# Performance work log

Hardware: AMD Instinct MI355X
Metric: run time of the kernel (lower is better)

The kernel has to match this reference:

```python
import jax, jax.numpy as jnp
import numpy as np

WH, WW = 16, 16
NUM_HEADS = 16
DIM = 1024
BATCH = 64
SEQ = WH * WW + 1  # 257, includes cls token
NUM_REL = (2 * WH - 1) * (2 * WW - 1) + 3  # 964


def _make_rel_pos_index(wh, ww):
    # BEiT relative position index construction (intended semantics of the torch code)
    coords = np.stack(np.meshgrid(np.arange(wh), np.arange(ww), indexing='ij'))  # [2, wh, ww]
    flat = coords.reshape(2, -1)  # [2, wh*ww]
    rel = flat[:, :, None] - flat[:, None, :]  # [2, N-1, N-1]
    rel = rel.transpose(1, 2, 0).astype(np.int64)
    rel[:, :, 0] += wh - 1
    rel[:, :, 1] += ww - 1
    rel[:, :, 0] *= 2 * ww - 1
    num_rel = (2 * wh - 1) * (2 * ww - 1) + 3
    idx = np.zeros((wh * ww + 1, wh * ww + 1), dtype=np.int32)
    idx[1:, 1:] = rel.sum(-1)
    idx[0, :] = num_rel - 3  # cls-to-token
    idx[:, 0] = num_rel - 2  # token-to-cls
    idx[0, 0] = num_rel - 1  # cls-to-cls
    return idx


def setup_inputs() -> dict:
    key = jax.random.key(0)
    ks = jax.random.split(key, 7)
    return {
        'x': jax.random.normal(ks[0], (BATCH, SEQ, DIM), dtype=jnp.float32),
        'qkv_weight': jax.random.normal(ks[1], (3 * DIM, DIM), dtype=jnp.float32) * 0.02,
        'query_bias': jax.random.normal(ks[2], (DIM,), dtype=jnp.float32) * 0.02,
        'value_bias': jax.random.normal(ks[3], (DIM,), dtype=jnp.float32) * 0.02,
        'rel_pos_bias_table': jax.random.normal(ks[4], (NUM_REL, NUM_HEADS), dtype=jnp.float32) * 0.02,
        'proj_weight': jax.random.normal(ks[5], (DIM, DIM), dtype=jnp.float32) * 0.02,
        'proj_bias': jax.random.normal(ks[6], (DIM,), dtype=jnp.float32) * 0.02,
        'rel_pos_index': jnp.asarray(_make_rel_pos_index(WH, WW)),
    }


def reference(x, qkv_weight, query_bias, value_bias, rel_pos_bias_table,
              proj_weight, proj_bias, rel_pos_index):
    B, N, C = x.shape
    H = rel_pos_bias_table.shape[-1]
    D = qkv_weight.shape[0] // 3 // H
    scale = D ** -0.5
    # qkv bias: (q_bias, zeros, v_bias) as in the torch module
    qkv_bias = jnp.concatenate([query_bias, jnp.zeros_like(value_bias), value_bias])
    qkv = x @ qkv_weight.T + qkv_bias  # [B, N, 3*H*D]
    qkv = qkv.reshape(B, N, 3, H, D).transpose(2, 0, 3, 1, 4)  # [3, B, H, N, D]
    q, k, v = qkv[0] * scale, qkv[1], qkv[2]
    attn = jnp.einsum('bhqd,bhkd->bhqk', q, k)  # [B, H, N, N]
    bias = rel_pos_bias_table[rel_pos_index]  # [N, N, H]
    attn = attn + bias.transpose(2, 0, 1)[None]  # add per-head bias
    attn = jax.nn.softmax(attn, axis=-1)
    out = jnp.einsum('bhqk,bhkd->bhqd', attn, v)  # [B, H, N, D]
    out = out.transpose(0, 2, 1, 3).reshape(B, N, H * D)
    return out @ proj_weight.T + proj_bias
```

## Files before the change

### kernel.cpp

```cpp
#include <hip/hip_runtime.h>


typedef unsigned short u16;
typedef __attribute__((ext_vector_type(8))) short bf16x8;
typedef __attribute__((ext_vector_type(4))) float f32x4;

#define MFMA16(a, b, c) __builtin_amdgcn_mfma_f32_16x16x32_bf16(a, b, c, 0, 0, 0)
#define GLDS16(g, l)                                                           \
  __builtin_amdgcn_global_load_lds(                                            \
      (const __attribute__((address_space(1))) void*)(g),                      \
      (__attribute__((address_space(3))) void*)(l), 16, 0, 0)

#define QOFF 0
#define KOFF 16842752
#define VTOFF 33685504
#define VTP 264

__device__ __forceinline__ u16 f2bf(float f) {
  unsigned u = __builtin_bit_cast(unsigned, f);
  u += 0x7FFFu + ((u >> 16) & 1u);
  return (u16)(u >> 16);
}
__device__ __forceinline__ unsigned pack2(float a, float b) {
  return (unsigned)f2bf(a) | ((unsigned)f2bf(b) << 16);
}

__global__ __launch_bounds__(256) void cvt_bf16(const float* __restrict__ in,
                                                u16* __restrict__ out, int n4) {
  int i = blockIdx.x * 256 + threadIdx.x;
  if (i < n4) {
    float4 v = ((const float4*)in)[i];
    uint2 o;
    o.x = pack2(v.x, v.y);
    o.y = pack2(v.z, v.w);
    ((uint2*)out)[i] = o;
  }
}

__global__ __launch_bounds__(256) void bias_pre(const float* __restrict__ tab,
                                                const int* __restrict__ idx,
                                                float* __restrict__ out) {
  int t = blockIdx.x * 256 + threadIdx.x;
  if (t < 66049) {
    int id = idx[t];
    const float* row = tab + (size_t)id * 16;
#pragma unroll
    for (int h = 0; h < 16; h++)
      out[(size_t)h * 66049 + t] = row[h] * 1.4426950408889634f;
  }
}


#define GEMM_PROLOG(M_, K_)                                                    \
  __shared__ __align__(16) u16 As[128 * 32];                                   \
  __shared__ __align__(16) u16 Bs[128 * 32];                                   \
  const int M = (M_), K = (K_);                                                \
  const int tid = threadIdx.x;                                                 \
  const int lane = tid & 63, wave = tid >> 6;                                  \
  const int quad = lane >> 4, l15 = lane & 15;                                 \
  const int wr = (wave >> 1) * 64, wc = (wave & 1) * 64;                       \
  const int m0 = blockIdx.y * 128, n0 = blockIdx.x * 128;                      \
  const int sgk = (((tid & 3) ^ ((tid >> 3) & 3))) * 8;  \
  const int fo = ((quad ^ ((l15 >> 1) & 3))) * 8;         \
  int ar0 = m0 + (tid >> 2); if (ar0 > M - 1) ar0 = M - 1;                     \
  int ar1 = m0 + 64 + (tid >> 2); if (ar1 > M - 1) ar1 = M - 1;                \
  const u16* pa0 = A + (size_t)ar0 * K + sgk;                                  \
  const u16* pa1 = A + (size_t)ar1 * K + sgk;                                  \
  const u16* pb0 = B + (size_t)(n0 + (tid >> 2)) * K + sgk;                    \
  const u16* pb1 = pb0 + (size_t)64 * K;                                       \
  f32x4 acc[4][4];                                                             \
  _Pragma("unroll") for (int i = 0; i < 4; i++)                                \
  _Pragma("unroll") for (int j = 0; j < 4; j++)                                \
      acc[i][j] = (f32x4){0.f, 0.f, 0.f, 0.f};                                 \
  for (int k0 = 0; k0 < K; k0 += 32) {                                         \
    __syncthreads();                                                           \
    GLDS16(pa0 + k0, As + tid * 8);                                            \
    GLDS16(pa1 + k0, As + 2048 + tid * 8);                                     \
    GLDS16(pb0 + k0, Bs + tid * 8);                                            \
    GLDS16(pb1 + k0, Bs + 2048 + tid * 8);                                     \
    __syncthreads();                                                           \
    bf16x8 af[4], bf[4];                                                       \
    _Pragma("unroll") for (int t = 0; t < 4; t++)                              \
        af[t] = *(const bf16x8*)(As + (wr + t * 16 + l15) * 32 + fo);          \
    _Pragma("unroll") for (int t = 0; t < 4; t++)                              \
        bf[t] = *(const bf16x8*)(Bs + (wc + t * 16 + l15) * 32 + fo);          \
    _Pragma("unroll") for (int i = 0; i < 4; i++)                              \
    _Pragma("unroll") for (int j = 0; j < 4; j++)                              \
        acc[i][j] = MFMA16(af[i], bf[j], acc[i][j]);                           \
  }

__global__ __launch_bounds__(256) void gemm_qkv(
    const u16* __restrict__ A, const u16* __restrict__ B,
    const float* __restrict__ qbias, const float* __restrict__ vbias,
    u16* __restrict__ C) {
  GEMM_PROLOG(16448, 1024)
#pragma unroll
  for (int i = 0; i < 4; i++) {
#pragma unroll
    for (int r = 0; r < 4; r++) {
      int row = m0 + wr + i * 16 + quad * 4 + r;
      if (row < M) {
        unsigned bb = (unsigned)row / 257u;
        unsigned nn = (unsigned)row - bb * 257u;
#pragma unroll
        for (int j = 0; j < 4; j++) {
          int c = n0 + wc + j * 16 + l15;
          int which = c >> 10, rem = c & 1023;
          float bias = (which == 0) ? qbias[rem]
                                    : ((which == 2) ? vbias[rem] : 0.f);
          float v = acc[i][j][r] + bias;
          if (which == 0) v *= 0.18033688011112042f;
          int h = rem >> 6, d = rem & 63;
          size_t dst;
          if (which == 2) {
            dst = (size_t)VTOFF + ((size_t)(bb * 16 + h) * 64 + d) * VTP + nn;
          } else {
            dst = (size_t)which * 16842752 + (size_t)(bb * 16 + h) * 16448 +
                  (size_t)nn * 64 + d;
          }
          C[dst] = f2bf(v);
        }
      }
    }
  }
}

__global__ __launch_bounds__(256) void gemm_proj(
    const u16* __restrict__ A, const u16* __restrict__ B,
    const float* __restrict__ pbias, float* __restrict__ C) {
  GEMM_PROLOG(16448, 1024)
#pragma unroll
  for (int i = 0; i < 4; i++) {
#pragma unroll
    for (int r = 0; r < 4; r++) {
      int row = m0 + wr + i * 16 + quad * 4 + r;
      if (row < M) {
#pragma unroll
        for (int j = 0; j < 4; j++) {
          int c = n0 + wc + j * 16 + l15;
          C[(size_t)row * 1024 + c] = acc[i][j][r] + pbias[c];
        }
      }
    }
  }
}

__global__ __launch_bounds__(256, 3) void attn_fused(
    const u16* __restrict__ qkv, const float* __restrict__ biasT,
    u16* __restrict__ out) {
  __shared__ __align__(16) u16 KVs[96 * 72];
  __shared__ __align__(16) u16 Ps[4 * 16 * 104];
  const int bx = blockIdx.x;
  const int qt = bx % 5, bh = bx / 5;
  const int b = bh >> 4, h = bh & 15;
  const int tid = threadIdx.x, lane = tid & 63, wave = tid >> 6;
  const int quad = lane >> 4, l15 = lane & 15;
  const u16* qg = qkv + QOFF + (size_t)bh * 16448;
  const u16* kg = qkv + KOFF + (size_t)bh * 16448;
  const u16* vtg = qkv + VTOFF + (size_t)bh * (64 * VTP);

  int qra = qt * 64 + wave * 16 + l15;
  if (qra > 256) qra = 256;
  const bf16x8 aq0 = *(const bf16x8*)(qg + (size_t)qra * 64 + quad * 8);
  const bf16x8 aq1 = *(const bf16x8*)(qg + (size_t)qra * 64 + 32 + quad * 8);

  const int qbase = qt * 64 + wave * 16 + quad * 4;
  const float* bb = biasT + (size_t)h * 66049;
  f32x4 s[18];
#pragma unroll
  for (int r = 0; r < 4; r++) {
    int qr = qbase + r;
    if (qr > 256) qr = 256;
    const float* brow = bb + (size_t)qr * 257;
#pragma unroll
    for (int t = 0; t < 18; t++) {
      int kc = t * 16 + l15;
      s[t][r] = (kc < 257) ? brow[kc] : -3e38f;
    }
  }

  const bf16x8 zv = {0, 0, 0, 0, 0, 0, 0, 0};
  for (int ck = 0; ck < 3; ck++) {
    __syncthreads();
#pragma unroll
    for (int it = 0; it < 3; it++) {
      int g = it * 256 + tid;
      int row = g >> 3, col = (g & 7) * 8;
      int gr = ck * 96 + row;
      bf16x8 kv = (gr < 257) ? *(const bf16x8*)(kg + (size_t)gr * 64 + col) : zv;
      *(bf16x8*)(KVs + row * 72 + col) = kv;
    }
    __syncthreads();
#pragma unroll
    for (int nt = 0; nt < 6; nt++) {
      bf16x8 b0 = *(const bf16x8*)(KVs + (nt * 16 + l15) * 72 + quad * 8);
      bf16x8 b1 = *(const bf16x8*)(KVs + (nt * 16 + l15) * 72 + 32 + quad * 8);
      int t = ck * 6 + nt;
      s[t] = MFMA16(aq0, b0, s[t]);
      s[t] = MFMA16(aq1, b1, s[t]);
    }
  }

  float inv[4];
#pragma unroll
  for (int r = 0; r < 4; r++) {
    float m = -3e38f;
#pragma unroll
    for (int t = 0; t < 18; t++) m = fmaxf(m, s[t][r]);
    m = fmaxf(m, __shfl_xor(m, 1));
    m = fmaxf(m, __shfl_xor(m, 2));
    m = fmaxf(m, __shfl_xor(m, 4));
    m = fmaxf(m, __shfl_xor(m, 8));
    float sum = 0.f;
#pragma unroll
    for (int t = 0; t < 18; t++) {
      float p = __builtin_amdgcn_exp2f(s[t][r] - m);
      s[t][r] = p;
      sum += p;
    }
    sum += __shfl_xor(sum, 1);
    sum += __shfl_xor(sum, 2);
    sum += __shfl_xor(sum, 4);
    sum += __shfl_xor(sum, 8);
    inv[r] = 1.f / sum;
  }

  u16* Pw = Ps + wave * (16 * 104);
  f32x4 o[4];
#pragma unroll
  for (int nt = 0; nt < 4; nt++) o[nt] = (f32x4){0.f, 0.f, 0.f, 0.f};
  for (int ck = 0; ck < 3; ck++) {
    __syncthreads();
#pragma unroll
    for (int it = 0; it < 3; it++) {
      int g = it * 256 + tid;
      int row = g / 12, c = (g % 12) * 8;
      bf16x8 v = *(const bf16x8*)(vtg + (size_t)row * VTP + ck * 96 + c);
      *(bf16x8*)(KVs + row * 104 + c) = v;
    }
#pragma unroll
    for (int nt = 0; nt < 6; nt++) {
      int t = ck * 6 + nt;
#pragma unroll
      for (int r = 0; r < 4; r++)
        Pw[(quad * 4 + r) * 104 + nt * 16 + l15] = f2bf(s[t][r]);
    }
    __syncthreads();
#pragma unroll
    for (int ks = 0; ks < 3; ks++) {
      bf16x8 ap = *(const bf16x8*)(Pw + l15 * 104 + ks * 32 + quad * 8);
#pragma unroll
      for (int nt = 0; nt < 4; nt++) {
        bf16x8 bv =
            *(const bf16x8*)(KVs + (nt * 16 + l15) * 104 + ks * 32 + quad * 8);
        o[nt] = MFMA16(ap, bv, o[nt]);
      }
    }
  }

#pragma unroll
  for (int nt = 0; nt < 4; nt++) {
    int d = nt * 16 + l15;
#pragma unroll
    for (int r = 0; r < 4; r++) {
      int qr = qbase + r;
      if (qr < 257)
        out[((size_t)b * 257 + qr) * 1024 + h * 64 + d] =
            f2bf(o[nt][r] * inv[r]);
    }
  }
}

extern "C" void kernel_launch(void* const* d_in, const int* in_sizes, int n_in,
                              void* d_out, int out_size, void* d_ws,
                              size_t ws_size, hipStream_t stream) {
  const float* x = (const float*)d_in[0];
  const float* qkvw = (const float*)d_in[1];
  const float* qb = (const float*)d_in[2];
  const float* vb = (const float*)d_in[3];
  const float* tab = (const float*)d_in[4];
  const float* pw = (const float*)d_in[5];
  const float* pb = (const float*)d_in[6];
  const int* rpi = (const int*)d_in[7];

  char* ws = (char*)d_ws;
  u16* qkvbuf = (u16*)ws;
  u16* xbuf = (u16*)(ws + 101974016);
  float* biasb = (float*)(ws + 135659520);
  u16* qkvwb = (u16*)(ws + 139886656);
  u16* projwb = (u16*)(ws + 146178112);

  cvt_bf16<<<16448, 256, 0, stream>>>(x, xbuf, 4210688);
  cvt_bf16<<<3072, 256, 0, stream>>>(qkvw, qkvwb, 786432);
  cvt_bf16<<<1024, 256, 0, stream>>>(pw, projwb, 262144);
  bias_pre<<<259, 256, 0, stream>>>(tab, rpi, biasb);
  gemm_qkv<<<dim3(24, 129), 256, 0, stream>>>(xbuf, qkvwb, qb, vb, qkvbuf);
  attn_fused<<<5120, 256, 0, stream>>>(qkvbuf, biasb, xbuf);
  gemm_proj<<<dim3(8, 129), 256, 0, stream>>>(xbuf, projwb, pb, (float*)d_out);
}
```

Measured before the change: 466.1 us.

## Double-buffer LDS tiles in QKV and projection GEMMs to overlap loads with MFMA

The shared GEMM main loop now uses two LDS buffers per operand. It issues the asynchronous global-to-LDS loads for the next K-slice before running the MFMAs on the current slice, so memory latency can hide behind compute instead of being serialized between barriers. The loop is unrolled by two over a fixed K of 1024, which drops the K parameter. This doubles the GEMM LDS footprint, which could lower occupancy.

Measured after the change: 474.7 us. No clear change (+1.8%).

```diff
diff --git a/kernel.cpp b/kernel.cpp
--- a/kernel.cpp
+++ b/kernel.cpp
@@ -51,10 +51,30 @@
 }
 
 
-#define GEMM_PROLOG(M_, K_)                                                    \
-  __shared__ __align__(16) u16 As[128 * 32];                                   \
-  __shared__ __align__(16) u16 Bs[128 * 32];                                   \
-  const int M = (M_), K = (K_);                                                \
+#define GEMM_PF(kof, bi)                                                       \
+  do {                                                                         \
+    GLDS16(pa0 + (kof), As[bi] + tid * 8);                                     \
+    GLDS16(pa1 + (kof), As[bi] + 2048 + tid * 8);                              \
+    GLDS16(pb0 + (kof), Bs[bi] + tid * 8);                                     \
+    GLDS16(pb1 + (kof), Bs[bi] + 2048 + tid * 8);                              \
+  } while (0)
+
+#define GEMM_STEP(bi)                                                          \
+  do {                                                                         \
+    bf16x8 af[4], bf[4];                                                       \
+    _Pragma("unroll") for (int t = 0; t < 4; t++)                              \
+        af[t] = *(const bf16x8*)(As[bi] + (wr + t * 16 + l15) * 32 + fo);      \
+    _Pragma("unroll") for (int t = 0; t < 4; t++)                              \
+        bf[t] = *(const bf16x8*)(Bs[bi] + (wc + t * 16 + l15) * 32 + fo);      \
+    _Pragma("unroll") for (int i = 0; i < 4; i++)                              \
+    _Pragma("unroll") for (int j = 0; j < 4; j++)                              \
+        acc[i][j] = MFMA16(af[i], bf[j], acc[i][j]);                           \
+  } while (0)
+
+#define GEMM_PROLOG(M_)                                                        \
+  __shared__ __align__(16) u16 As[2][128 * 32];                                \
+  __shared__ __align__(16) u16 Bs[2][128 * 32];                                \
+  const int M = (M_);                                                          \
   const int tid = threadIdx.x;                                                 \
   const int lane = tid & 63, wave = tid >> 6;                                  \
   const int quad = lane >> 4, l15 = lane & 15;                                 \
@@ -64,36 +84,30 @@
   const int fo = ((quad ^ ((l15 >> 1) & 3))) * 8;         \
   int ar0 = m0 + (tid >> 2); if (ar0 > M - 1) ar0 = M - 1;                     \
   int ar1 = m0 + 64 + (tid >> 2); if (ar1 > M - 1) ar1 = M - 1;                \
-  const u16* pa0 = A + (size_t)ar0 * K + sgk;                                  \
-  const u16* pa1 = A + (size_t)ar1 * K + sgk;                                  \
-  const u16* pb0 = B + (size_t)(n0 + (tid >> 2)) * K + sgk;                    \
-  const u16* pb1 = pb0 + (size_t)64 * K;                                       \
+  const u16* pa0 = A + (size_t)ar0 * 1024 + sgk;                               \
+  const u16* pa1 = A + (size_t)ar1 * 1024 + sgk;                               \
+  const u16* pb0 = B + (size_t)(n0 + (tid >> 2)) * 1024 + sgk;                 \
+  const u16* pb1 = pb0 + (size_t)64 * 1024;                                    \
   f32x4 acc[4][4];                                                             \
   _Pragma("unroll") for (int i = 0; i < 4; i++)                                \
   _Pragma("unroll") for (int j = 0; j < 4; j++)                                \
       acc[i][j] = (f32x4){0.f, 0.f, 0.f, 0.f};                                 \
-  for (int k0 = 0; k0 < K; k0 += 32) {                                         \
-    __syncthreads();                                                           \
-    GLDS16(pa0 + k0, As + tid * 8);                                            \
-    GLDS16(pa1 + k0, As + 2048 + tid * 8);                                     \
-    GLDS16(pb0 + k0, Bs + tid * 8);                                            \
-    GLDS16(pb1 + k0, Bs + 2048 + tid * 8);                                     \
-    __syncthreads();                                                           \
-    bf16x8 af[4], bf[4];                                                       \
-    _Pragma("unroll") for (int t = 0; t < 4; t++)                              \
-        af[t] = *(const bf16x8*)(As + (wr + t * 16 + l15) * 32 + fo);          \
-    _Pragma("unroll") for (int t = 0; t < 4; t++)                              \
-        bf[t] = *(const bf16x8*)(Bs + (wc + t * 16 + l15) * 32 + fo);          \
-    _Pragma("unroll") for (int i = 0; i < 4; i++)                              \
-    _Pragma("unroll") for (int j = 0; j < 4; j++)                              \
-        acc[i][j] = MFMA16(af[i], bf[j], acc[i][j]);                           \
+  GEMM_PF(0, 0);                                                               \
+  for (int t = 0; t < 16; t++) {                                               \
+    int k1 = t * 64 + 32;                                                      \
+    __syncthreads();            \
+    GEMM_PF(k1, 1);                                                            \
+    GEMM_STEP(0);                                                              \
+    __syncthreads();            \
+    if (t < 15) GEMM_PF(k1 + 32, 0);                                           \
+    GEMM_STEP(1);                                                              \
   }
 
 __global__ __launch_bounds__(256) void gemm_qkv(
     const u16* __restrict__ A, const u16* __restrict__ B,
     const float* __restrict__ qbias, const float* __restrict__ vbias,
     u16* __restrict__ C) {
-  GEMM_PROLOG(16448, 1024)
+  GEMM_PROLOG(16448)
 #pragma unroll
   for (int i = 0; i < 4; i++) {
 #pragma unroll
@@ -128,7 +142,7 @@
 __global__ __launch_bounds__(256) void gemm_proj(
     const u16* __restrict__ A, const u16* __restrict__ B,
     const float* __restrict__ pbias, float* __restrict__ C) {
-  GEMM_PROLOG(16448, 1024)
+  GEMM_PROLOG(16448)
 #pragma unroll
   for (int i = 0; i < 4; i++) {
 #pragma unroll
```
